# Kernel optimization log

Measured on AMD Instinct MI355X. Metric: run time of the kernel, lower is better.

Reference implementation:

```python
import jax, jax.numpy as jnp
import numpy as np

EPS = 1e-5

def _conv3x3(x, w, stride=1):
    # x: [N,C,H,W], w: [O,I,3,3], padding=1
    return jax.lax.conv_general_dilated(
        x, w,
        window_strides=(stride, stride),
        padding=((1, 1), (1, 1)),
        dimension_numbers=("NCHW", "OIHW", "NCHW"),
    )

def _bn(x, gamma, beta, mean, var):
    # inference-mode BatchNorm2d with running stats; per-channel over C of NCHW
    inv = gamma * jax.lax.rsqrt(var + EPS)
    return x * inv[None, :, None, None] + (beta - mean * inv)[None, :, None, None]

def setup_inputs() -> dict:
    key = jax.random.key(0)
    ks = jax.random.split(key, 11)
    N, C, H, W = 32, 256, 56, 56
    x = jax.random.normal(ks[0], (N, C, H, W), dtype=jnp.float32)
    fan = C * 9
    w1 = jax.random.normal(ks[1], (C, C, 3, 3), dtype=jnp.float32) / np.sqrt(fan)
    w2 = jax.random.normal(ks[2], (C, C, 3, 3), dtype=jnp.float32) / np.sqrt(fan)
    g1 = jax.random.uniform(ks[3], (C,), dtype=jnp.float32, minval=0.5, maxval=1.5)
    b1 = jax.random.normal(ks[4], (C,), dtype=jnp.float32) * 0.1
    m1 = jax.random.normal(ks[5], (C,), dtype=jnp.float32) * 0.1
    v1 = jax.random.uniform(ks[6], (C,), dtype=jnp.float32, minval=0.5, maxval=1.5)
    g2 = jax.random.uniform(ks[7], (C,), dtype=jnp.float32, minval=0.5, maxval=1.5)
    b2 = jax.random.normal(ks[8], (C,), dtype=jnp.float32) * 0.1
    m2 = jax.random.normal(ks[9], (C,), dtype=jnp.float32) * 0.1
    v2 = jax.random.uniform(ks[10], (C,), dtype=jnp.float32, minval=0.5, maxval=1.5)
    return {"x": x, "w1": w1, "g1": g1, "b1": b1, "m1": m1, "v1": v1,
            "w2": w2, "g2": g2, "b2": b2, "m2": m2, "v2": v2}

def reference(x, w1, g1, b1, m1, v1, w2, g2, b2, m2, v2):
    identity = x
    out = jax.nn.relu(_bn(_conv3x3(x, w1, stride=1), g1, b1, m1, v1))
    out = _bn(_conv3x3(out, w2, stride=1), g2, b2, m2, v2)
    return jax.nn.relu(out + identity)
```

## Files before the change

### kernel.cpp

```cpp
#include <hip/hip_runtime.h>
#include <hip/hip_bf16.h>


typedef __attribute__((ext_vector_type(8))) short bf16x8;
typedef __attribute__((ext_vector_type(4))) float f32x4;
typedef __attribute__((ext_vector_type(4))) unsigned int uint4v;

#define C_CH   256
#define HW_IMG 3136
#define CHW    802816
#define WELEM  589824
#define RSTR   40
#define BUFE   7680
#define NCH    8
#define NSTEP  72
#define ZROW   15360

__device__ __forceinline__ ushort f2bf(float f){
    union{__hip_bfloat16 h; ushort u;} c; c.h = __float2bfloat16(f); return c.u;
}

__global__ __launch_bounds__(256) void prep_kernel(
    const float* __restrict__ w1, const float* __restrict__ w2,
    const float* __restrict__ g1, const float* __restrict__ b1,
    const float* __restrict__ m1, const float* __restrict__ v1,
    const float* __restrict__ g2, const float* __restrict__ b2,
    const float* __restrict__ m2, const float* __restrict__ v2,
    ushort* __restrict__ wf1, ushort* __restrict__ wf2,
    float* __restrict__ bn, ushort* __restrict__ zb)
{
    int gid = blockIdx.x * 256 + threadIdx.x;
    if (gid < WELEM) {
        int j = gid & 7, l = (gid >> 3) & 63, ct = (gid >> 9) & 15, rr = gid >> 13;
        int c = rr / 9, r = rr - c * 9;
        int co = ct * 16 + (l & 15);
        int ci = c * 32 + (l >> 4) * 8 + j;
        wf1[gid] = f2bf(w1[(co * C_CH + ci) * 9 + r]);
    }
    int g2i = gid - WELEM;
    if (g2i >= 0 && g2i < WELEM) {
        int j = g2i & 7, l = (g2i >> 3) & 63, ct = (g2i >> 9) & 15, rr = g2i >> 13;
        int c = rr / 9, r = rr - c * 9;
        int co = ct * 16 + (l & 15);
        int ci = c * 32 + (l >> 4) * 8 + j;
        wf2[g2i] = f2bf(w2[(co * C_CH + ci) * 9 + r]);
    }
    if (gid < C_CH) {
        float i1 = g1[gid] * rsqrtf(v1[gid] + 1e-5f);
        bn[gid]            = i1;
        bn[C_CH + gid]     = b1[gid] - m1[gid] * i1;
        float i2 = g2[gid] * rsqrtf(v2[gid] + 1e-5f);
        bn[2*C_CH + gid]   = i2;
        bn[3*C_CH + gid]   = b2[gid] - m2[gid] * i2;
    }
    if (gid < 512) zb[gid] = 0;
}

__global__ __launch_bounds__(256) void xpose_kernel(
    const float* __restrict__ x, ushort* __restrict__ xT)
{
    __shared__ ushort T[64 * 72];
    int tid = threadIdx.x;
    int b = blockIdx.x;
    int n = b / 196, rem = b % 196;
    int pb = rem >> 2, cb = rem & 3;
    int lane = tid & 63, cr = tid >> 6;
    const float* xp = x + ((size_t)(n * C_CH + cb * 64)) * HW_IMG + pb * 64 + lane;
#pragma unroll
    for (int j = 0; j < 16; ++j) {
        int cil = cr * 16 + j;
        T[lane * 72 + cil] = f2bf(xp[(size_t)cil * HW_IMG]);
    }
    __syncthreads();
#pragma unroll
    for (int it = 0; it < 2; ++it) {
        int slot = it * 256 + tid;
        int p = slot >> 3, g = slot & 7;
        uint4v v = *(const uint4v*)&T[p * 72 + g * 8];
        *(uint4v*)(xT + ((size_t)n * HW_IMG + pb * 64 + p) * C_CH + cb * 64 + g * 8) = v;
    }
}

#define READB(dst, bufE, s)                                                  \
    {                                                                        \
        const int dw_ = (s) % 3 - 1;                                         \
        const int off_ = ((s) / 3 - 1) * 56 * RSTR + dw_ * RSTR + (bufE);    \
        _Pragma("unroll")                                                    \
        for (int nc_ = 0; nc_ < 4; ++nc_) {                                  \
            bool ok_ = (dw_ == -1) ? wLa[nc_]                                \
                                   : ((dw_ == 1) ? wRa[nc_] : true);         \
            int idx_ = ok_ ? (vbe[nc_] + off_) : zidx;                       \
            dst[nc_] = *(const bf16x8*)&B[idx_];                             \
        }                                                                    \
    }

#define MFMA16(bq, t)                                                        \
    __builtin_amdgcn_s_setprio(1);                                           \
    _Pragma("unroll")                                                        \
    for (int mr_ = 0; mr_ < 4; ++mr_) {                                      \
        _Pragma("unroll")                                                    \
        for (int nc_ = 0; nc_ < 4; ++nc_)                                    \
            acc[mr_][nc_] = __builtin_amdgcn_mfma_f32_16x16x32_bf16(         \
                areg[(t) & 1][mr_], bq[nc_], acc[mr_][nc_], 0, 0, 0);        \
    }                                                                        \
    __builtin_amdgcn_s_setprio(0);

template<bool SECOND>
__global__ __launch_bounds__(256, 2) void conv_kernel(
    const ushort* __restrict__ srcT,
    const ushort* __restrict__ wf,
    const float* __restrict__ bnp,
    const float* __restrict__ ident,
    const ushort* __restrict__ zb,
    void* __restrict__ dst)
{
    __shared__ ushort B[16896];

    const int tid = threadIdx.x;
    const int wv = tid >> 6, l = tid & 63;
    const int lr = l & 15, lg = l >> 4;

    int bid = blockIdx.x;
    int swz = (bid & 7) * 196 + (bid >> 3);
    const int n = swz / 49, pt = swz % 49;
    const int p0 = pt * 64;

    bool wLa[4], wRa[4];
    int vbe[4];
#pragma unroll
    for (int nc = 0; nc < 4; ++nc) {
        int p = p0 + nc * 16 + lr;
        int w = p % 56;
        wLa[nc] = (w > 0);
        wRa[nc] = (w < 55);
        vbe[nc] = (64 + nc * 16 + lr) * RSTR + lg * 8;
    }
    const int zidx = ZROW + lg * 8;

    const ushort* sA[4];
#pragma unroll
    for (int rd = 0; rd < 4; ++rd) {
        int slot = rd * 256 + tid;
        int row = slot / 5, g = slot - row * 5;
        int gp = p0 - 64 + row;
        bool val = (g < 4) && (gp >= 0) && (gp < HW_IMG) && (slot < 960);
        sA[rd] = val ? (srcT + ((size_t)n * HW_IMG + gp) * C_CH + g * 8)
                     : (zb + g * 8);
    }

    auto stage = [&](int cix, int bufE) {
#pragma unroll
        for (int rd = 0; rd < 4; ++rd) {
            if (rd < 3 || tid < 192) {
                __builtin_amdgcn_global_load_lds(
                    (const __attribute__((address_space(1))) void*)(sA[rd] + cix * 32),
                    (__attribute__((address_space(3))) void*)&B[bufE + (rd * 256 + tid) * 8],
                    16, 0, 0);
            }
        }
    };

    f32x4 acc[4][4];
#pragma unroll
    for (int mr = 0; mr < 4; ++mr)
#pragma unroll
        for (int nc = 0; nc < 4; ++nc) {
            f32x4 z = {0.f, 0.f, 0.f, 0.f};
            acc[mr][nc] = z;
        }

    bf16x8 areg[2][4];
    const ushort* pWb = wf + wv * 2048 + l * 8;

    auto loadA = [&](int t, bf16x8* a) {
#pragma unroll
        for (int mr = 0; mr < 4; ++mr)
            a[mr] = *(const bf16x8*)(pWb + t * 8192 + mr * 512);
    };

    stage(0, 0);
    if (tid < 40) B[ZROW + tid] = 0;
    loadA(0, areg[0]);
    __syncthreads();

#pragma unroll
    for (int c = 0; c < NCH; ++c) {
        const int bufE = (c & 1) ? BUFE : 0;
        bf16x8 bqA[4], bqB[4];
        READB(bqA, bufE, 0);
#pragma unroll
        for (int s = 0; s < 9; ++s) {
            const int t = c * 9 + s;
            if (t + 1 < NSTEP) loadA(t + 1, areg[(t + 1) & 1]);
            if (s == 3 && c + 1 < NCH) stage(c + 1, bufE ^ BUFE);
            if ((s & 1) == 0) {
                if (s + 1 < 9) READB(bqB, bufE, s + 1);
                MFMA16(bqA, t);
            } else {
                READB(bqA, bufE, s + 1);
                MFMA16(bqB, t);
            }
        }
        __syncthreads();
    }

    if constexpr (!SECOND) {
        ushort* T = B;
#pragma unroll
        for (int mr = 0; mr < 4; ++mr) {
#pragma unroll
            for (int nc = 0; nc < 4; ++nc) {
                int co0 = wv * 64 + mr * 16 + lg * 4;
                float v0 = fmaxf(acc[mr][nc][0] * bnp[co0+0] + bnp[C_CH+co0+0], 0.f);
                float v1 = fmaxf(acc[mr][nc][1] * bnp[co0+1] + bnp[C_CH+co0+1], 0.f);
                float v2 = fmaxf(acc[mr][nc][2] * bnp[co0+2] + bnp[C_CH+co0+2], 0.f);
                float v3 = fmaxf(acc[mr][nc][3] * bnp[co0+3] + bnp[C_CH+co0+3], 0.f);
                uint2 pk;
                pk.x = (uint)f2bf(v0) | ((uint)f2bf(v1) << 16);
                pk.y = (uint)f2bf(v2) | ((uint)f2bf(v3) << 16);
                *(uint2*)&T[(nc * 16 + lr) * 264 + co0] = pk;
            }
        }
        __syncthreads();
        ushort* yT = (ushort*)dst;
#pragma unroll
        for (int it = 0; it < 8; ++it) {
            int slot = it * 256 + tid;
            int row = slot >> 5, g = slot & 31;
            uint4v v = *(const uint4v*)&T[row * 264 + g * 8];
            *(uint4v*)(yT + ((size_t)n * HW_IMG + p0 + row) * C_CH + g * 8) = v;
        }
    } else {
        const size_t nbase = (size_t)n * CHW;
        float* out = (float*)dst;
#pragma unroll
        for (int mr = 0; mr < 4; ++mr) {
#pragma unroll
            for (int nc = 0; nc < 4; ++nc) {
                int pc = p0 + nc * 16 + lr;
#pragma unroll
                for (int i = 0; i < 4; ++i) {
                    int co = wv * 64 + mr * 16 + lg * 4 + i;
                    size_t o = nbase + (size_t)co * HW_IMG + pc;
                    float val = acc[mr][nc][i] * bnp[co] + bnp[C_CH + co] + ident[o];
                    out[o] = fmaxf(val, 0.f);
                }
            }
        }
    }
}

extern "C" void kernel_launch(void* const* d_in, const int* in_sizes, int n_in,
                              void* d_out, int out_size, void* d_ws, size_t ws_size,
                              hipStream_t stream) {
    const float* x  = (const float*)d_in[0];
    const float* w1 = (const float*)d_in[1];
    const float* g1 = (const float*)d_in[2];
    const float* b1 = (const float*)d_in[3];
    const float* m1 = (const float*)d_in[4];
    const float* v1 = (const float*)d_in[5];
    const float* w2 = (const float*)d_in[6];
    const float* g2 = (const float*)d_in[7];
    const float* b2 = (const float*)d_in[8];
    const float* m2 = (const float*)d_in[9];
    const float* v2 = (const float*)d_in[10];

    ushort* wf1 = (ushort*)d_ws;
    ushort* wf2 = wf1 + WELEM;
    float*  bn  = (float*)(wf2 + WELEM);
    ushort* zb  = (ushort*)(bn + 4 * C_CH);
    ushort* yT  = zb + 512;
    ushort* xT  = (ushort*)d_out;

    prep_kernel<<<dim3(4608), dim3(256), 0, stream>>>(
        w1, w2, g1, b1, m1, v1, g2, b2, m2, v2, wf1, wf2, bn, zb);

    xpose_kernel<<<dim3(6272), dim3(256), 0, stream>>>(x, xT);

    conv_kernel<false><<<dim3(1568), dim3(256), 0, stream>>>(
        xT, wf1, bn, x, zb, (void*)yT);

    conv_kernel<true><<<dim3(1568), dim3(256), 0, stream>>>(
        yT, wf2, bn + 512, x, zb, d_out);
}
```

Before: 256.0 us.

## Split conv output tile across two channel halves for higher occupancy

Each conv block now computes 128 output channels × 64 pixels instead of 256×64, with its four waves arranged 2×2 over channels and pixels. The grid doubles to 3136 blocks and launch bounds ask for 4 blocks per CU, halving accumulator registers per thread. The aim is more occupancy and better latency hiding. In exchange, the input pixel tile is staged into LDS twice, once per channel half, so input global and LDS traffic doubles and each B fragment feeds fewer MFMAs.

```diff
diff --git a/kernel.cpp b/kernel.cpp
--- a/kernel.cpp
+++ b/kernel.cpp
@@ -15,6 +15,7 @@
 #define NCH    8
 #define NSTEP  72
 #define ZROW   15360
+#define TSTR   136
 
 __device__ __forceinline__ ushort f2bf(float f){
     union{__hip_bfloat16 h; ushort u;} c; c.h = __float2bfloat16(f); return c.u;
@@ -86,7 +87,7 @@
         const int dw_ = (s) % 3 - 1;                                         \
         const int off_ = ((s) / 3 - 1) * 56 * RSTR + dw_ * RSTR + (bufE);    \
         _Pragma("unroll")                                                    \
-        for (int nc_ = 0; nc_ < 4; ++nc_) {                                  \
+        for (int nc_ = 0; nc_ < 2; ++nc_) {                                  \
             bool ok_ = (dw_ == -1) ? wLa[nc_]                                \
                                    : ((dw_ == 1) ? wRa[nc_] : true);         \
             int idx_ = ok_ ? (vbe[nc_] + off_) : zidx;                       \
@@ -94,19 +95,19 @@
         }                                                                    \
     }
 
-#define MFMA16(bq, t)                                                        \
+#define MFMA8(bq, t)                                                         \
     __builtin_amdgcn_s_setprio(1);                                           \
     _Pragma("unroll")                                                        \
     for (int mr_ = 0; mr_ < 4; ++mr_) {                                      \
         _Pragma("unroll")                                                    \
-        for (int nc_ = 0; nc_ < 4; ++nc_)                                    \
+        for (int nc_ = 0; nc_ < 2; ++nc_)                                    \
             acc[mr_][nc_] = __builtin_amdgcn_mfma_f32_16x16x32_bf16(         \
                 areg[(t) & 1][mr_], bq[nc_], acc[mr_][nc_], 0, 0, 0);        \
     }                                                                        \
     __builtin_amdgcn_s_setprio(0);
 
 template<bool SECOND>
-__global__ __launch_bounds__(256, 2) void conv_kernel(
+__global__ __launch_bounds__(256, 4) void conv_kernel(
     const ushort* __restrict__ srcT,
     const ushort* __restrict__ wf,
     const float* __restrict__ bnp,
@@ -118,22 +119,25 @@
 
     const int tid = threadIdx.x;
     const int wv = tid >> 6, l = tid & 63;
+    const int wm = wv & 1, wn = wv >> 1;
     const int lr = l & 15, lg = l >> 4;
 
     int bid = blockIdx.x;
-    int swz = (bid & 7) * 196 + (bid >> 3);
-    const int n = swz / 49, pt = swz % 49;
+    int swz = (bid & 7) * 392 + (bid >> 3);
+    const int n  = swz / 98;
+    const int r98 = swz - n * 98;
+    const int pt = r98 >> 1, cb = r98 & 1;
     const int p0 = pt * 64;
 
-    bool wLa[4], wRa[4];
-    int vbe[4];
-#pragma unroll
-    for (int nc = 0; nc < 4; ++nc) {
-        int p = p0 + nc * 16 + lr;
+    bool wLa[2], wRa[2];
+    int vbe[2];
+#pragma unroll
+    for (int nc = 0; nc < 2; ++nc) {
+        int p = p0 + wn * 32 + nc * 16 + lr;
         int w = p % 56;
         wLa[nc] = (w > 0);
         wRa[nc] = (w < 55);
-        vbe[nc] = (64 + nc * 16 + lr) * RSTR + lg * 8;
+        vbe[nc] = (64 + wn * 32 + nc * 16 + lr) * RSTR + lg * 8;
     }
     const int zidx = ZROW + lg * 8;
 
@@ -160,17 +164,17 @@
         }
     };
 
-    f32x4 acc[4][4];
+    f32x4 acc[4][2];
 #pragma unroll
     for (int mr = 0; mr < 4; ++mr)
 #pragma unroll
-        for (int nc = 0; nc < 4; ++nc) {
+        for (int nc = 0; nc < 2; ++nc) {
             f32x4 z = {0.f, 0.f, 0.f, 0.f};
             acc[mr][nc] = z;
         }
 
     bf16x8 areg[2][4];
-    const ushort* pWb = wf + wv * 2048 + l * 8;
+    const ushort* pWb = wf + cb * 4096 + wm * 2048 + l * 8;
 
     auto loadA = [&](int t, bf16x8* a) {
 #pragma unroll
@@ -186,7 +190,7 @@
 #pragma unroll
     for (int c = 0; c < NCH; ++c) {
         const int bufE = (c & 1) ? BUFE : 0;
-        bf16x8 bqA[4], bqB[4];
+        bf16x8 bqA[2], bqB[2];
         READB(bqA, bufE, 0);
 #pragma unroll
         for (int s = 0; s < 9; ++s) {
@@ -195,10 +199,10 @@
             if (s == 3 && c + 1 < NCH) stage(c + 1, bufE ^ BUFE);
             if ((s & 1) == 0) {
                 if (s + 1 < 9) READB(bqB, bufE, s + 1);
-                MFMA16(bqA, t);
+                MFMA8(bqA, t);
             } else {
                 READB(bqA, bufE, s + 1);
-                MFMA16(bqB, t);
+                MFMA8(bqB, t);
             }
         }
         __syncthreads();
@@ -209,26 +213,28 @@
 #pragma unroll
         for (int mr = 0; mr < 4; ++mr) {
 #pragma unroll
-            for (int nc = 0; nc < 4; ++nc) {
-                int co0 = wv * 64 + mr * 16 + lg * 4;
-                float v0 = fmaxf(acc[mr][nc][0] * bnp[co0+0] + bnp[C_CH+co0+0], 0.f);
-                float v1 = fmaxf(acc[mr][nc][1] * bnp[co0+1] + bnp[C_CH+co0+1], 0.f);
-                float v2 = fmaxf(acc[mr][nc][2] * bnp[co0+2] + bnp[C_CH+co0+2], 0.f);
-                float v3 = fmaxf(acc[mr][nc][3] * bnp[co0+3] + bnp[C_CH+co0+3], 0.f);
+            for (int nc = 0; nc < 2; ++nc) {
+                int col = wm * 64 + mr * 16 + lg * 4;
+                int cog = cb * 128 + col;
+                int row = wn * 32 + nc * 16 + lr;
+                float v0 = fmaxf(acc[mr][nc][0] * bnp[cog+0] + bnp[C_CH+cog+0], 0.f);
+                float v1 = fmaxf(acc[mr][nc][1] * bnp[cog+1] + bnp[C_CH+cog+1], 0.f);
+                float v2 = fmaxf(acc[mr][nc][2] * bnp[cog+2] + bnp[C_CH+cog+2], 0.f);
+                float v3 = fmaxf(acc[mr][nc][3] * bnp[cog+3] + bnp[C_CH+cog+3], 0.f);
                 uint2 pk;
                 pk.x = (uint)f2bf(v0) | ((uint)f2bf(v1) << 16);
                 pk.y = (uint)f2bf(v2) | ((uint)f2bf(v3) << 16);
-                *(uint2*)&T[(nc * 16 + lr) * 264 + co0] = pk;
+                *(uint2*)&T[row * TSTR + col] = pk;
             }
         }
         __syncthreads();
         ushort* yT = (ushort*)dst;
 #pragma unroll
-        for (int it = 0; it < 8; ++it) {
+        for (int it = 0; it < 4; ++it) {
             int slot = it * 256 + tid;
-            int row = slot >> 5, g = slot & 31;
-            uint4v v = *(const uint4v*)&T[row * 264 + g * 8];
-            *(uint4v*)(yT + ((size_t)n * HW_IMG + p0 + row) * C_CH + g * 8) = v;
+            int row = slot >> 4, g = slot & 15;
+            uint4v v = *(const uint4v*)&T[row * TSTR + g * 8];
+            *(uint4v*)(yT + ((size_t)n * HW_IMG + p0 + row) * C_CH + cb * 128 + g * 8) = v;
         }
     } else {
         const size_t nbase = (size_t)n * CHW;
@@ -236,11 +242,11 @@
 #pragma unroll
         for (int mr = 0; mr < 4; ++mr) {
 #pragma unroll
-            for (int nc = 0; nc < 4; ++nc) {
-                int pc = p0 + nc * 16 + lr;
+            for (int nc = 0; nc < 2; ++nc) {
+                int pc = p0 + wn * 32 + nc * 16 + lr;
 #pragma unroll
                 for (int i = 0; i < 4; ++i) {
-                    int co = wv * 64 + mr * 16 + lg * 4 + i;
+                    int co = cb * 128 + wm * 64 + mr * 16 + lg * 4 + i;
                     size_t o = nbase + (size_t)co * HW_IMG + pc;
                     float val = acc[mr][nc][i] * bnp[co] + bnp[C_CH + co] + ident[o];
                     out[o] = fmaxf(val, 0.f);
@@ -277,9 +283,9 @@
 
     xpose_kernel<<<dim3(6272), dim3(256), 0, stream>>>(x, xT);
 
-    conv_kernel<false><<<dim3(1568), dim3(256), 0, stream>>>(
+    conv_kernel<false><<<dim3(3136), dim3(256), 0, stream>>>(
         xT, wf1, bn, x, zb, (void*)yT);
 
-    conv_kernel<true><<<dim3(1568), dim3(256), 0, stream>>>(
+    conv_kernel<true><<<dim3(3136), dim3(256), 0, stream>>>(
         yT, wf2, bn + 512, x, zb, d_out);
 }
```

Measured after the change: 339.0 us. 32.4% more time.
